# Kernel optimization log

Hardware: AMD Instinct MI355X
Metric: run time of the kernel (lower is better)

The kernel has to match this reference:

```python
import jax, jax.numpy as jnp
import numpy as np

DIM = 512
MAXP = 100
N_SAMPLED = MAXP - 2  # partitions 0 (whole) and 1 (singletons) handled analytically
KMAX = 6              # sampled partitions have 2..6 parts


def _make_part_masks(dim, n_sampled, kmax, seed=0):
    rng = np.random.default_rng(seed)
    masks = np.zeros((n_sampled, kmax, dim), dtype=bool)
    for p in range(n_sampled):
        n_parts = rng.integers(2, kmax + 1)
        assign = rng.integers(0, n_parts, size=dim)
        for k in range(n_parts):
            masks[p, k] = assign == k
    return masks


def setup_inputs() -> dict:
    key = jax.random.key(0)
    ks = jax.random.split(key, 10)
    B, S, D = 8, 4096, DIM
    x = jax.random.normal(ks[0], (B, S, D), dtype=jnp.float32)
    entropy_scales = jnp.ones((D,), dtype=jnp.float32)
    integration_weights = jnp.ones((MAXP,), dtype=jnp.float32)
    W1 = jax.random.normal(ks[1], (32, 1), dtype=jnp.float32) * 0.5
    b1 = jax.random.normal(ks[2], (32,), dtype=jnp.float32) * 0.1
    W2 = jax.random.normal(ks[3], (16, 32), dtype=jnp.float32) * 0.2
    b2 = jax.random.normal(ks[4], (16,), dtype=jnp.float32) * 0.1
    W3 = jax.random.normal(ks[5], (1, 16), dtype=jnp.float32) * 0.3
    b3 = jax.random.normal(ks[6], (1,), dtype=jnp.float32) * 0.1
    part_masks = jnp.asarray(_make_part_masks(D, N_SAMPLED, KMAX))  # [P,K,D] bool
    return {"x": x, "entropy_scales": entropy_scales,
            "integration_weights": integration_weights,
            "W1": W1, "b1": b1, "W2": W2, "b2": b2, "W3": W3, "b3": b3,
            "part_masks": part_masks}


def _phi(x, entropy_scales, integration_weights, W1, b1, W2, b2, W3, b3, part_masks):
    B, S, D = x.shape
    # ---- full-flatten entropy (per batch), H(softmax(x.reshape(B,-1))) ----
    lp = jax.nn.log_softmax(x.reshape(B, -1), axis=-1)
    H_full = -jnp.sum(jnp.exp(lp) * lp, axis=-1)                     # [B]
    h_full_scaled = H_full * entropy_scales.mean()                   # [B]
    h_whole = H_full.mean()                                          # partition idx 0

    # ---- singleton partition (idx 1): softmax over seq per (b,d) ----
    lps = jax.nn.log_softmax(x, axis=1)                              # [B,S,D]
    H_sd = -jnp.sum(jnp.exp(lps) * lps, axis=1)                      # [B,D]
    h_single = H_sd.mean(axis=0).sum()

    # ---- sampled partitions via masks: per part, softmax over (seq x part dims) ----
    xmax_d = x.max(axis=1)                                           # [B,D]
    ex = jnp.exp(x - xmax_d[:, None, :])                             # [B,S,D]
    e_d = ex.sum(axis=1)                                             # [B,D] sum exp(x - xmax_d)
    t_d = (ex * x).sum(axis=1)                                       # [B,D] sum exp(.)*x
    valid = part_masks.any(axis=-1)                                  # [P,K]
    neg = jnp.finfo(x.dtype).min
    gmax = jnp.max(jnp.where(part_masks[None], xmax_d[:, None, None, :], neg), axis=-1)  # [B,P,K]
    gmax = jnp.where(valid[None], gmax, 0.0)
    shift = jnp.exp(xmax_d[:, None, None, :] - gmax[..., None])      # [B,P,K,D] <= 1
    mf = part_masks.astype(x.dtype)
    Z = jnp.einsum('pkd,bd,bpkd->bpk', mf, e_d, shift)               # group partition fn
    T = jnp.einsum('pkd,bd,bpkd->bpk', mf, t_d, shift)
    Zs = jnp.where(valid[None], Z, 1.0)
    H_pk = gmax + jnp.log(Zs) - T / Zs                               # group entropy [B,P,K]
    H_pk = jnp.where(valid[None], H_pk, 0.0)
    h_sampled = H_pk.mean(axis=0).sum(axis=-1)                       # [P] sum of part entropies

    h_parts = jnp.concatenate([jnp.stack([h_whole, h_single]), h_sampled])   # [100]
    weighted = h_parts * jax.nn.sigmoid(integration_weights[: h_parts.shape[0]])
    min_part = weighted.min()

    raw_phi = h_full_scaled.mean() - min_part
    z = jnp.clip(raw_phi / 10.0, 0.0, 1.0)[None]                     # [1]
    h = jax.nn.relu(z @ W1.T + b1)
    h = jax.nn.relu(h @ W2.T + b2)
    conf = jax.nn.sigmoid(h @ W3.T + b3).squeeze(-1)                 # scalar
    return conf


def reference(x, entropy_scales, integration_weights, W1, b1, W2, b2, W3, b3, part_masks):
    return _phi(x, entropy_scales, integration_weights, W1, b1, W2, b2, W3, b3, part_masks)
```

## Files before the change

kernel.cpp:

```cpp
#include <hip/hip_runtime.h>
#include <math.h>

constexpr int Bv = 8;
constexpr int Sv = 4096;
constexpr int Dv = 512;
constexpr int NCv = 64;
constexpr int SCv = Sv / NCv;
constexpr int Pv = 98;
constexpr int Kv = 6;
constexpr int MAXPv = 100;

typedef float v4f __attribute__((ext_vector_type(4)));

constexpr size_t OFF_ZPART = 0;
constexpr size_t OFF_TPART = OFF_ZPART + (size_t)Bv * NCv * Dv;
constexpr size_t OFF_ZD    = OFF_TPART + (size_t)Bv * NCv * Dv;
constexpr size_t OFF_TD    = OFF_ZD + (size_t)Bv * Dv;
constexpr size_t OFF_HFULL = OFF_TD + (size_t)Bv * Dv;
constexpr size_t OFF_HSD   = OFF_HFULL + Bv;
constexpr size_t OFF_HBP   = OFF_HSD + Bv;

__device__ __forceinline__ float warpSum(float v) {
    for (int o = 32; o > 0; o >>= 1) v += __shfl_xor(v, o);
    return v;
}
__device__ __forceinline__ float blockSum512(float v, float* red) {
    float s = warpSum(v);
    int lane = threadIdx.x & 63, w = threadIdx.x >> 6;
    __syncthreads();
    if (lane == 0) red[w] = s;
    __syncthreads();
    return red[0] + red[1] + red[2] + red[3] + red[4] + red[5] + red[6] + red[7];
}

__device__ __forceinline__ float sigmoidf(float v) { return 1.0f / (1.0f + __expf(-v)); }

__device__ __forceinline__ v4f exp4(v4f v) {
    v4f e;
    e.x = __expf(v.x); e.y = __expf(v.y); e.z = __expf(v.z); e.w = __expf(v.w);
    return e;
}

__global__ __launch_bounds__(512) void k1_partial(const float* __restrict__ x,
                                                  float* __restrict__ ws) {
    int c = blockIdx.x;
    int b = blockIdx.y;
    int tid = threadIdx.x;
    int dg = tid & 127;
    int sl = tid >> 7;

    const v4f* xv = (const v4f*)x;
    v4f z = (v4f){0.f, 0.f, 0.f, 0.f};
    v4f t = (v4f){0.f, 0.f, 0.f, 0.f};

    int sbase = c * SCv + sl;
#pragma unroll 8
    for (int i = 0; i < SCv / 4; i++) {
        int s = sbase + 4 * i;
        v4f v = __builtin_nontemporal_load(&xv[((size_t)b * Sv + s) * 128 + dg]);
        v4f e = exp4(v);
        z += e;
        t += e * v;
    }

    __shared__ v4f smz[256], smt[256];
    if (sl & 1) {
        int base = (sl >> 1) * 128 + dg;
        smz[base] = z; smt[base] = t;
    }
    __syncthreads();
    if (!(sl & 1)) {
        int base = (sl >> 1) * 128 + dg;
        z += smz[base]; t += smt[base];
    }
    __syncthreads();
    if (sl == 2) {
        smz[dg] = z; smt[dg] = t;
    }
    __syncthreads();
    if (sl == 0) {
        z += smz[dg]; t += smt[dg];
        size_t o = ((size_t)(b * NCv + c)) * 128 + dg;
        ((v4f*)(ws + OFF_ZPART))[o] = z;
        ((v4f*)(ws + OFF_TPART))[o] = t;
    }
}

__global__ __launch_bounds__(512) void k2_combine(float* __restrict__ ws) {
    int b = blockIdx.x;
    int tid = threadIdx.x;
    int dg = tid & 127;
    int ci = tid >> 7;

    const v4f* zp = (const v4f*)(ws + OFF_ZPART);
    const v4f* tp = (const v4f*)(ws + OFF_TPART);

    v4f z = (v4f){0.f, 0.f, 0.f, 0.f};
    v4f t = (v4f){0.f, 0.f, 0.f, 0.f};

#pragma unroll 8
    for (int i = 0; i < NCv / 4; i++) {
        int c = ci + 4 * i;
        size_t o = ((size_t)(b * NCv + c)) * 128 + dg;
        z += zp[o];
        t += tp[o];
    }

    __shared__ v4f smz[256], smt[256];
    __shared__ float red[8];
    if (ci & 1) {
        int base = (ci >> 1) * 128 + dg;
        smz[base] = z; smt[base] = t;
    }
    __syncthreads();
    if (!(ci & 1)) {
        int base = (ci >> 1) * 128 + dg;
        z += smz[base]; t += smt[base];
    }
    __syncthreads();
    if (ci == 2) {
        smz[dg] = z; smt[dg] = t;
    }
    __syncthreads();

    float hsd_part = 0.f;
    float zc = 0.f, tc = 0.f;
    if (ci == 0) {
        z += smz[dg]; t += smt[dg];

        size_t o = (size_t)b * 128 + dg;
        ((v4f*)(ws + OFF_ZD))[o] = z;
        ((v4f*)(ws + OFF_TD))[o] = t;

        hsd_part = (__logf(z.x) - t.x / z.x) + (__logf(z.y) - t.y / z.y) +
                   (__logf(z.z) - t.z / z.z) + (__logf(z.w) - t.w / z.w);
        zc = z.x + z.y + z.z + z.w;
        tc = t.x + t.y + t.z + t.w;
    }

    float sum_h = blockSum512(hsd_part, red);
    float zb = blockSum512(zc, red);
    float tb = blockSum512(tc, red);
    if (tid == 0) {
        ws[OFF_HSD + b] = sum_h;
        ws[OFF_HFULL + b] = __logf(zb) - tb / zb;
    }
}

__global__ __launch_bounds__(512) void k3_parts(const void* __restrict__ masks,
                                                float* __restrict__ ws) {
    int p = blockIdx.x;
    int b = blockIdx.y;
    int d = threadIdx.x;
    int lane = d & 63, w = d >> 6;

    __shared__ int f;
    if (d == 0) f = 0;
    __syncthreads();
    if (((const unsigned int*)masks)[d] > 1u) f = 1;
    __syncthreads();

    int mk = 255;
    if (f) {
        const unsigned char* mbyt = (const unsigned char*)masks;
        for (int k = 0; k < Kv; k++)
            if (mbyt[((size_t)p * Kv + k) * Dv + d]) { mk = k; break; }
    } else {
        const int* mint = (const int*)masks;
        for (int k = 0; k < Kv; k++)
            if (mint[((size_t)p * Kv + k) * Dv + d]) { mk = k; break; }
    }

    float z = ws[OFF_ZD + (size_t)b * Dv + d];
    float t = ws[OFF_TD + (size_t)b * Dv + d];

    __shared__ float lz[8 * Kv], lt[8 * Kv];
    __shared__ float hk[Kv];

    for (int k = 0; k < Kv; k++) {
        float cz = (mk == k) ? z : 0.f;
        float ct = (mk == k) ? t : 0.f;
        float sz = warpSum(cz);
        float st = warpSum(ct);
        if (lane == 0) { lz[w * Kv + k] = sz; lt[w * Kv + k] = st; }
    }
    __syncthreads();
    if (d < Kv) {
        float Z = 0.f, T = 0.f;
        for (int ww = 0; ww < 8; ww++) { Z += lz[ww * Kv + d]; T += lt[ww * Kv + d]; }
        hk[d] = (Z > 0.f) ? __logf(Z) - T / Z : 0.f;
    }
    __syncthreads();
    if (d == 0)
        ws[OFF_HBP + (size_t)b * Pv + p] =
            hk[0] + hk[1] + hk[2] + hk[3] + hk[4] + hk[5];
}

__global__ __launch_bounds__(128) void k4_final(
    const float* __restrict__ es, const float* __restrict__ iw,
    const float* __restrict__ W1, const float* __restrict__ b1,
    const float* __restrict__ W2, const float* __restrict__ b2,
    const float* __restrict__ W3, const float* __restrict__ b3,
    const float* __restrict__ ws, float* __restrict__ out) {
    int tid = threadIdx.x;
    __shared__ float wgt[MAXPv];
    __shared__ float meanH_s;
    __shared__ float red[2];

    float v = es[tid] + es[tid + 128] + es[tid + 256] + es[tid + 384];
    float s64 = warpSum(v);
    int lane = tid & 63, w = tid >> 6;
    if (lane == 0) red[w] = s64;
    __syncthreads();
    float es_mean = (red[0] + red[1]) * (1.0f / 512.0f);

    if (tid < Pv) {
        float s = 0.f;
        for (int b = 0; b < Bv; b++) s += ws[OFF_HBP + (size_t)b * Pv + tid];
        wgt[tid + 2] = (s * (1.0f / Bv)) * sigmoidf(iw[tid + 2]);
    } else if (tid == Pv) {
        float s = 0.f;
        for (int b = 0; b < Bv; b++) s += ws[OFF_HFULL + b];
        float mh = s * (1.0f / Bv);
        meanH_s = mh;
        wgt[0] = mh * sigmoidf(iw[0]);
    } else if (tid == Pv + 1) {
        float s = 0.f;
        for (int b = 0; b < Bv; b++) s += ws[OFF_HSD + b];
        wgt[1] = (s * (1.0f / Bv)) * sigmoidf(iw[1]);
    }
    __syncthreads();

    if (tid == 0) {
        float mn = wgt[0];
        for (int i = 1; i < MAXPv; i++) mn = fminf(mn, wgt[i]);
        float raw = es_mean * meanH_s - mn;
        float z = fminf(fmaxf(raw * 0.1f, 0.0f), 1.0f);

        float h1[32];
        for (int j = 0; j < 32; j++) {
            float a = z * W1[j] + b1[j];
            h1[j] = a > 0.f ? a : 0.f;
        }
        float h2[16];
        for (int i = 0; i < 16; i++) {
            float a = b2[i];
            for (int j = 0; j < 32; j++) a += W2[i * 32 + j] * h1[j];
            h2[i] = a > 0.f ? a : 0.f;
        }
        float a = b3[0];
        for (int i = 0; i < 16; i++) a += W3[i] * h2[i];
        out[0] = sigmoidf(a);
    }
}

extern "C" void kernel_launch(void* const* d_in, const int* in_sizes, int n_in,
                              void* d_out, int out_size, void* d_ws, size_t ws_size,
                              hipStream_t stream) {
    const float* x  = (const float*)d_in[0];
    const float* es = (const float*)d_in[1];
    const float* iw = (const float*)d_in[2];
    const float* W1 = (const float*)d_in[3];
    const float* b1 = (const float*)d_in[4];
    const float* W2 = (const float*)d_in[5];
    const float* b2 = (const float*)d_in[6];
    const float* W3 = (const float*)d_in[7];
    const float* b3 = (const float*)d_in[8];
    const void* masks = d_in[9];
    float* ws = (float*)d_ws;
    float* out = (float*)d_out;

    k1_partial<<<dim3(NCv, Bv), dim3(512), 0, stream>>>(x, ws);
    k2_combine<<<dim3(Bv), dim3(512), 0, stream>>>(ws);
    k3_parts<<<dim3(Pv, Bv), dim3(512), 0, stream>>>(masks, ws);
    k4_final<<<dim3(1), dim3(128), 0, stream>>>(es, iw, W1, b1, W2, b2, W3, b3, ws, out);
}
```

Measured before the change: 137.9 us.

## Spread combine stage over more blocks and move per-batch entropy reductions to final kernel

The combine kernel now runs on an 8x8 grid, with each block handling a 16-column slice of d, instead of 8 blocks each reducing all 64 chunks. That gives it far more parallelism on a tiny stage. The per-batch singleton and full entropies, which needed block-wide reductions, move into the single-block final kernel, now 512 threads, which reads the z/t arrays directly. The first kernel's intra-block reduction is also flattened to a single sync. The trade-off is extra serial work in the final kernel.

```diff
diff --git a/kernel.cpp b/kernel.cpp
--- a/kernel.cpp
+++ b/kernel.cpp
@@ -16,21 +16,11 @@
 constexpr size_t OFF_TPART = OFF_ZPART + (size_t)Bv * NCv * Dv;
 constexpr size_t OFF_ZD    = OFF_TPART + (size_t)Bv * NCv * Dv;
 constexpr size_t OFF_TD    = OFF_ZD + (size_t)Bv * Dv;
-constexpr size_t OFF_HFULL = OFF_TD + (size_t)Bv * Dv;
-constexpr size_t OFF_HSD   = OFF_HFULL + Bv;
-constexpr size_t OFF_HBP   = OFF_HSD + Bv;
+constexpr size_t OFF_HBP   = OFF_TD + (size_t)Bv * Dv;
 
 __device__ __forceinline__ float warpSum(float v) {
     for (int o = 32; o > 0; o >>= 1) v += __shfl_xor(v, o);
     return v;
-}
-__device__ __forceinline__ float blockSum512(float v, float* red) {
-    float s = warpSum(v);
-    int lane = threadIdx.x & 63, w = threadIdx.x >> 6;
-    __syncthreads();
-    if (lane == 0) red[w] = s;
-    __syncthreads();
-    return red[0] + red[1] + red[2] + red[3] + red[4] + red[5] + red[6] + red[7];
 }
 
 __device__ __forceinline__ float sigmoidf(float v) { return 1.0f / (1.0f + __expf(-v)); }
@@ -63,23 +53,15 @@
         t += e * v;
     }
 
-    __shared__ v4f smz[256], smt[256];
-    if (sl & 1) {
-        int base = (sl >> 1) * 128 + dg;
-        smz[base] = z; smt[base] = t;
-    }
-    __syncthreads();
-    if (!(sl & 1)) {
-        int base = (sl >> 1) * 128 + dg;
-        z += smz[base]; t += smt[base];
-    }
-    __syncthreads();
-    if (sl == 2) {
-        smz[dg] = z; smt[dg] = t;
+    __shared__ v4f smz[3][128], smt[3][128];
+    if (sl) {
+        smz[sl - 1][dg] = z;
+        smt[sl - 1][dg] = t;
     }
     __syncthreads();
     if (sl == 0) {
-        z += smz[dg]; t += smt[dg];
+        z += smz[0][dg] + smz[1][dg] + smz[2][dg];
+        t += smt[0][dg] + smt[1][dg] + smt[2][dg];
         size_t o = ((size_t)(b * NCv + c)) * 128 + dg;
         ((v4f*)(ws + OFF_ZPART))[o] = z;
         ((v4f*)(ws + OFF_TPART))[o] = t;
@@ -87,63 +69,42 @@
 }
 
 __global__ __launch_bounds__(512) void k2_combine(float* __restrict__ ws) {
-    int b = blockIdx.x;
+    int slice = blockIdx.x;
+    int b = blockIdx.y;
     int tid = threadIdx.x;
-    int dg = tid & 127;
-    int ci = tid >> 7;
+    int dgl = tid & 15;
+    int ci = tid >> 4;
+    int dg = slice * 16 + dgl;
 
     const v4f* zp = (const v4f*)(ws + OFF_ZPART);
     const v4f* tp = (const v4f*)(ws + OFF_TPART);
 
-    v4f z = (v4f){0.f, 0.f, 0.f, 0.f};
-    v4f t = (v4f){0.f, 0.f, 0.f, 0.f};
-
-#pragma unroll 8
-    for (int i = 0; i < NCv / 4; i++) {
-        int c = ci + 4 * i;
-        size_t o = ((size_t)(b * NCv + c)) * 128 + dg;
-        z += zp[o];
-        t += tp[o];
-    }
-
-    __shared__ v4f smz[256], smt[256];
-    __shared__ float red[8];
-    if (ci & 1) {
-        int base = (ci >> 1) * 128 + dg;
-        smz[base] = z; smt[base] = t;
-    }
-    __syncthreads();
-    if (!(ci & 1)) {
-        int base = (ci >> 1) * 128 + dg;
-        z += smz[base]; t += smt[base];
-    }
-    __syncthreads();
-    if (ci == 2) {
-        smz[dg] = z; smt[dg] = t;
-    }
-    __syncthreads();
-
-    float hsd_part = 0.f;
-    float zc = 0.f, tc = 0.f;
+    size_t base = (size_t)b * NCv * 128 + dg;
+    size_t o0 = base + (size_t)ci * 128;
+    size_t o1 = o0 + (size_t)32 * 128;
+    v4f z = zp[o0] + zp[o1];
+    v4f t = tp[o0] + tp[o1];
+
+    __shared__ v4f smz[32][16], smt[32][16];
+    smz[ci][dgl] = z;
+    smt[ci][dgl] = t;
+    __syncthreads();
+    if (ci < 4) {
+#pragma unroll
+        for (int j = 1; j < 8; j++) {
+            z += smz[ci + 4 * j][dgl];
+            t += smt[ci + 4 * j][dgl];
+        }
+        smz[ci][dgl] = z;
+        smt[ci][dgl] = t;
+    }
+    __syncthreads();
     if (ci == 0) {
-        z += smz[dg]; t += smt[dg];
-
+        z += smz[1][dgl] + smz[2][dgl] + smz[3][dgl];
+        t += smt[1][dgl] + smt[2][dgl] + smt[3][dgl];
         size_t o = (size_t)b * 128 + dg;
         ((v4f*)(ws + OFF_ZD))[o] = z;
         ((v4f*)(ws + OFF_TD))[o] = t;
-
-        hsd_part = (__logf(z.x) - t.x / z.x) + (__logf(z.y) - t.y / z.y) +
-                   (__logf(z.z) - t.z / z.z) + (__logf(z.w) - t.w / z.w);
-        zc = z.x + z.y + z.z + z.w;
-        tc = t.x + t.y + t.z + t.w;
-    }
-
-    float sum_h = blockSum512(hsd_part, red);
-    float zb = blockSum512(zc, red);
-    float tb = blockSum512(tc, red);
-    if (tid == 0) {
-        ws[OFF_HSD + b] = sum_h;
-        ws[OFF_HFULL + b] = __logf(zb) - tb / zb;
     }
 }
 
@@ -196,23 +157,46 @@
             hk[0] + hk[1] + hk[2] + hk[3] + hk[4] + hk[5];
 }
 
-__global__ __launch_bounds__(128) void k4_final(
+__global__ __launch_bounds__(512) void k4_final(
     const float* __restrict__ es, const float* __restrict__ iw,
     const float* __restrict__ W1, const float* __restrict__ b1,
     const float* __restrict__ W2, const float* __restrict__ b2,
     const float* __restrict__ W3, const float* __restrict__ b3,
     const float* __restrict__ ws, float* __restrict__ out) {
     int tid = threadIdx.x;
+    int lane = tid & 63, w = tid >> 6;
+    __shared__ float red[8];
+    __shared__ float perb[8][Bv][3];
+    __shared__ float hsd_sh[Bv], hfull_sh[Bv];
     __shared__ float wgt[MAXPv];
     __shared__ float meanH_s;
-    __shared__ float red[2];
-
-    float v = es[tid] + es[tid + 128] + es[tid + 256] + es[tid + 384];
-    float s64 = warpSum(v);
-    int lane = tid & 63, w = tid >> 6;
+
+    float s64 = warpSum(es[tid]);
     if (lane == 0) red[w] = s64;
-    __syncthreads();
-    float es_mean = (red[0] + red[1]) * (1.0f / 512.0f);
+
+    for (int b = 0; b < Bv; b++) {
+        float z = ws[OFF_ZD + (size_t)b * Dv + tid];
+        float t = ws[OFF_TD + (size_t)b * Dv + tid];
+        float h = __logf(z) - t / z;
+        float hs = warpSum(h);
+        float zs = warpSum(z);
+        float ts = warpSum(t);
+        if (lane == 0) { perb[w][b][0] = hs; perb[w][b][1] = zs; perb[w][b][2] = ts; }
+    }
+    __syncthreads();
+    float es_mean = (red[0] + red[1] + red[2] + red[3] +
+                     red[4] + red[5] + red[6] + red[7]) * (1.0f / 512.0f);
+    if (tid < Bv) {
+        float hs = 0.f, zs = 0.f, ts = 0.f;
+        for (int ww = 0; ww < 8; ww++) {
+            hs += perb[ww][tid][0];
+            zs += perb[ww][tid][1];
+            ts += perb[ww][tid][2];
+        }
+        hsd_sh[tid] = hs;
+        hfull_sh[tid] = __logf(zs) - ts / zs;
+    }
+    __syncthreads();
 
     if (tid < Pv) {
         float s = 0.f;
@@ -220,13 +204,13 @@
         wgt[tid + 2] = (s * (1.0f / Bv)) * sigmoidf(iw[tid + 2]);
     } else if (tid == Pv) {
         float s = 0.f;
-        for (int b = 0; b < Bv; b++) s += ws[OFF_HFULL + b];
+        for (int b = 0; b < Bv; b++) s += hfull_sh[b];
         float mh = s * (1.0f / Bv);
         meanH_s = mh;
         wgt[0] = mh * sigmoidf(iw[0]);
     } else if (tid == Pv + 1) {
         float s = 0.f;
-        for (int b = 0; b < Bv; b++) s += ws[OFF_HSD + b];
+        for (int b = 0; b < Bv; b++) s += hsd_sh[b];
         wgt[1] = (s * (1.0f / Bv)) * sigmoidf(iw[1]);
     }
     __syncthreads();
@@ -271,7 +255,7 @@
     float* out = (float*)d_out;
 
     k1_partial<<<dim3(NCv, Bv), dim3(512), 0, stream>>>(x, ws);
-    k2_combine<<<dim3(Bv), dim3(512), 0, stream>>>(ws);
+    k2_combine<<<dim3(8, Bv), dim3(512), 0, stream>>>(ws);
     k3_parts<<<dim3(Pv, Bv), dim3(512), 0, stream>>>(masks, ws);
-    k4_final<<<dim3(1), dim3(128), 0, stream>>>(es, iw, W1, b1, W2, b2, W3, b3, ws, out);
-}
+    k4_final<<<dim3(1), dim3(512), 0, stream>>>(es, iw, W1, b1, W2, b2, W3, b3, ws, out);
+}
```

Measured after the change: 141.6 us. 1.03x slower.
